# Kernel tuning notes

Hardware: AMD Instinct MI355X
Metric: run time of the kernel (lower is better)

## Reference

```python
import jax, jax.numpy as jnp
import numpy as np

BS, N, K, H = 32, 512, 32, 64

def _lin(k, i, o):
    return jax.random.normal(k, (i, o), jnp.float32) / np.sqrt(i).astype(np.float32)

def setup_inputs() -> dict:
    key = jax.random.key(0)
    ks = jax.random.split(key, 16)
    return {
        "ped_features": jax.random.normal(ks[0], (BS, N, 6), jnp.float32),
        "h_st": jax.random.normal(ks[1], (BS, N, H), jnp.float32),
        "h_neigh": jax.random.normal(ks[2], (BS, N, K, H), jnp.float32),
        "rela_features": jax.random.normal(ks[3], (BS, N, K, 6), jnp.float32),
        "neigh_mask": jax.random.randint(ks[4], (BS, N, K), 0, 2).astype(bool),
        "we1_w": _lin(ks[5], 2 * H + 1, H), "we1_b": jnp.zeros((H,), jnp.float32),
        "we2_w": _lin(ks[6], H, H),         "we2_b": jnp.zeros((H,), jnp.float32),
        "wx1_w": _lin(ks[7], H, H),         "wx1_b": jnp.zeros((H,), jnp.float32),
        "wx2_w": _lin(ks[8], H, 2),         "wx2_b": jnp.zeros((2,), jnp.float32),
        "wa_w":  _lin(ks[9], H, 2),         "wa_b":  jnp.zeros((2,), jnp.float32),
        "wh1_w": _lin(ks[10], 2 * H, H),    "wh1_b": jnp.zeros((H,), jnp.float32),
        "wh2_w": _lin(ks[11], H, H),        "wh2_b": jnp.zeros((H,), jnp.float32),
    }

def reference(ped_features, h_st, h_neigh, rela_features, neigh_mask,
              we1_w, we1_b, we2_w, we2_b,
              wx1_w, wx1_b, wx2_w, wx2_b,
              wa_w, wa_b, wh1_w, wh1_b, wh2_w, wh2_b):
    silu = jax.nn.silu
    # pairwise distances from relative positions  [bs,N,k]
    dists = jnp.sqrt(jnp.sum(rela_features[..., :2] ** 2, axis=-1))
    neigh_num = neigh_mask.sum(axis=-1).astype(h_st.dtype)  # [bs,N]
    # edge features: [h_i repeated, h_j, dist]  -> [bs,N,k,2H+1]
    h_rep = jnp.broadcast_to(h_st[:, :, None, :], (BS, N, K, H))
    tmp = jnp.concatenate([h_rep, h_neigh, dists[..., None]], axis=-1)
    # f_e
    m_ij = silu(silu(tmp @ we1_w + we1_b) @ we2_w + we2_b)  # [bs,N,k,H]
    # f_x -> per-edge 2-vector gates
    fx = silu(silu(m_ij @ wx1_w + wx1_b) @ wx2_w + wx2_b)   # [bs,N,k,2]
    agg = rela_features[..., :2] * fx
    agg = jnp.where(neigh_mask[..., None], agg, 0.0)
    agg = agg.sum(axis=-2) / (neigh_num[..., None] + 1e-6)  # masked mean [bs,N,2]
    # f_a node acceleration update
    a_new = silu(h_st @ wa_w + wa_b) * ped_features[..., 4:] + agg
    v_new = ped_features[..., 2:4] + a_new
    x_new = ped_features[..., :2] + v_new
    # message sum + f_h residual hidden update
    m_i = m_ij.sum(axis=-2)  # [bs,N,H]
    h_new = h_st + (silu(jnp.concatenate([h_st, m_i], axis=-1) @ wh1_w + wh1_b) @ wh2_w + wh2_b)
    return jnp.concatenate([x_new, v_new, a_new], axis=-1), h_new
```

## Files before the change

kernel.cpp:

```cpp
#include <hip/hip_runtime.h>

#define KK 32
#define NODES 16384
#define NPB 16
#define NPWV 4

typedef __bf16 bf16x8 __attribute__((ext_vector_type(8)));
typedef float  f32x4  __attribute__((ext_vector_type(4)));

union FragU { uint4 u; bf16x8 b; unsigned short s[8]; };

__device__ inline float bf2f(unsigned short v) {
    union { unsigned int u; float f; } t; t.u = ((unsigned int)v) << 16; return t.f;
}
__device__ inline unsigned short f2bf(float f) {
    union { float f; unsigned int u; } t; t.f = f;
    unsigned int u = t.u;
    return (unsigned short)((u + 0x7FFFu + ((u >> 16) & 1u)) >> 16);
}
__device__ inline unsigned int pkbf(float a, float b) {
    return (unsigned int)f2bf(a) | ((unsigned int)f2bf(b) << 16);
}
__device__ inline float silu_f(float x) { return x / (1.0f + __expf(-x)); }

__device__ inline float loadf(const void* p, int f32f, int idx) {
    return f32f ? ((const float*)p)[idx] : bf2f(((const unsigned short*)p)[idx]);
}
__device__ inline bf16x8 load8(const void* p, int f32f, int idx) {
    if (f32f) {
        const float* s = (const float*)p + idx;
        float4 lo = *(const float4*)s;
        float4 hi = *(const float4*)(s + 4);
        bf16x8 t;
        t[0] = (__bf16)lo.x; t[1] = (__bf16)lo.y; t[2] = (__bf16)lo.z; t[3] = (__bf16)lo.w;
        t[4] = (__bf16)hi.x; t[5] = (__bf16)hi.y; t[6] = (__bf16)hi.z; t[7] = (__bf16)hi.w;
        return t;
    }
    FragU t; t.u = *(const uint4*)((const unsigned short*)p + idx);
    return t.b;
}
__device__ inline int read_mask(const void* p, int flag, int i) {
    if (flag == 1) return ((const int*)p)[i] != 0;
    if (flag == 0) return ((const unsigned char*)p)[i] != 0;
    if (flag == 2) return ((const unsigned short*)p)[i] != 0;
    return ((const float*)p)[i] != 0.0f;
}
__device__ inline void fence_lds() {
    __builtin_amdgcn_sched_barrier(0);
    __builtin_amdgcn_wave_barrier();
    __builtin_amdgcn_sched_barrier(0);
}

__global__ __launch_bounds__(256, 2) void fused_kernel(
    const void* __restrict__ ped,   const void* __restrict__ h_st,
    const void* __restrict__ h_neigh, const void* __restrict__ rela,
    const void* __restrict__ maskp,
    const void* __restrict__ we1_w, const void* __restrict__ we1_b,
    const void* __restrict__ we2_w, const void* __restrict__ we2_b,
    const void* __restrict__ wx1_w, const void* __restrict__ wx1_b,
    const void* __restrict__ wx2_w, const void* __restrict__ wx2_b,
    const void* __restrict__ wa_w,  const void* __restrict__ wa_b,
    const void* __restrict__ wh1_w, const void* __restrict__ wh1_b,
    const void* __restrict__ wh2_w, const void* __restrict__ wh2_b,
    float* __restrict__ out0, float* __restrict__ out1)
{
    __shared__ uint4 wfr[44][64];
    __shared__ __align__(16) unsigned int lbuf[4][2][16][36];
    __shared__ __align__(16) unsigned int mibuf[16][36];
    __shared__ __align__(16) unsigned int abuf[16][36];
    __shared__ float aggbuf[16][2];
    __shared__ int flagsh[2];

    const int tid  = threadIdx.x;
    const int lane = tid & 63, wv = tid >> 6;
    const int q = lane >> 4, cl = lane & 15;

    if (wv == 0) {
        const unsigned short* hh = (const unsigned short*)h_st;
        bool ok = true;
        #pragma unroll
        for (int t = 0; t < 2; t++) {
            unsigned short v = hh[lane*2 + t];
            if (v) { int e = (v >> 7) & 0xFF; if (e < 90 || e > 165) ok = false; }
        }
        unsigned long long bm = __ballot(ok);
        const unsigned int*   mw = (const unsigned int*)maskp;
        const unsigned short* mh = (const unsigned short*)maskp;
        bool w01 = mw[lane] <= 1u;
        unsigned short h0 = mh[lane*2], h1 = mh[lane*2 + 1];
        bool s16 = (h0 == 0 || h0 == 0x3F80u) && (h1 == 0 || h1 == 0x3F80u);
        bool enz = (h0 != 0);
        unsigned long long bw = __ballot(w01);
        unsigned long long bs = __ballot(s16);
        unsigned long long be = __ballot(enz);
        if (lane == 0) {
            flagsh[1] = (bm == ~0ULL) ? 0 : 1;
            int mf;
            if (bw == ~0ULL) mf = 1;
            else if (bs == ~0ULL) mf = be ? 2 : 3;
            else mf = 0;
            flagsh[0] = mf;
        }
    }
    __syncthreads();
    const int mflag = flagsh[0], f32f = flagsh[1];

    for (int idx = tid; idx < 44*64; idx += 256) {
        int f = idx >> 6, l = idx & 63;
        int lq = l >> 4, ln = l & 15;
        const void *W, *B; int g, klim;
        if (f < 20)      { g = f;      W = we1_w; B = we1_b; klim = 129; }
        else if (f < 32) { g = f - 20; W = we2_w; B = we2_b; klim = 64; }
        else             { g = f - 32; W = wx1_w; B = wx1_b; klim = 64; }
        int ks = g >> 2, nt = g & 3;
        int n = nt*16 + ln;
        FragU fr;
        #pragma unroll
        for (int j = 0; j < 8; j++) {
            int k = ks*32 + lq*8 + j;
            float v = (k < klim) ? loadf(W, f32f, k*64 + n)
                                 : (k == klim ? loadf(B, f32f, n) : 0.0f);
            fr.s[j] = f2bf(v);
        }
        wfr[f][l] = fr.u;
    }
    __syncthreads();

    float wx2r0[4][4], wx2r1[4][4];
    #pragma unroll
    for (int nt = 0; nt < 4; nt++)
        #pragma unroll
        for (int rr = 0; rr < 4; rr++) {
            int frow = nt*16 + q*4 + rr;
            wx2r0[nt][rr] = loadf(wx2_w, f32f, frow*2);
            wx2r1[nt][rr] = loadf(wx2_w, f32f, frow*2 + 1);
        }
    const float bx20 = loadf(wx2_b, f32f, 0), bx21 = loadf(wx2_b, f32f, 1);
    const f32x4 zz = {0.f, 0.f, 0.f, 0.f};

    FragU bc;
    #pragma unroll
    for (int j = 0; j < 8; j++) bc.s[j] = 0;
    if (q == 0) bc.s[0] = 0x3F80u;

    #pragma unroll 1
    for (int it = 0; it < NPWV; ++it) {
        const int node = blockIdx.x*NPB + wv*NPWV + it;

        bf16x8 bst[2];
        #pragma unroll
        for (int ks = 0; ks < 2; ks++)
            bst[ks] = load8(h_st, f32f, node*64 + ks*32 + q*8);
        bf16x8 bng[2][2];
        #pragma unroll
        for (int et = 0; et < 2; et++)
            #pragma unroll
            for (int ks = 0; ks < 2; ks++)
                bng[et][ks] = load8(h_neigh, f32f, (node*KK + et*16 + cl)*64 + ks*32 + q*8);

        float rx[2], ry[2], dv[2]; int mk[2];
        #pragma unroll
        for (int et = 0; et < 2; et++) {
            int e = node*KK + et*16 + cl;
            rx[et] = loadf(rela, f32f, e*6);
            ry[et] = loadf(rela, f32f, e*6 + 1);
            dv[et] = sqrtf(rx[et]*rx[et] + ry[et]*ry[et]);
            mk[et] = read_mask(maskp, mflag, e);
        }
        FragU bext[2];
        #pragma unroll
        for (int et = 0; et < 2; et++) {
            #pragma unroll
            for (int j = 0; j < 8; j++) bext[et].s[j] = 0;
            if (q == 0) { bext[et].s[0] = f2bf(dv[et]); bext[et].s[1] = 0x3F80u; }
        }

        f32x4 acc[2][4];
        #pragma unroll
        for (int et = 0; et < 2; et++)
            #pragma unroll
            for (int nt = 0; nt < 4; nt++) acc[et][nt] = zz;
        #pragma unroll
        for (int ks = 0; ks < 5; ks++) {
            bf16x8 b0 = (ks < 2) ? bst[ks] : (ks < 4 ? bng[0][ks-2] : bext[0].b);
            bf16x8 b1 = (ks < 2) ? bst[ks] : (ks < 4 ? bng[1][ks-2] : bext[1].b);
            #pragma unroll
            for (int nt = 0; nt < 4; nt++) {
                FragU w; w.u = wfr[ks*4 + nt][lane];
                acc[0][nt] = __builtin_amdgcn_mfma_f32_16x16x32_bf16(w.b, b0, acc[0][nt], 0, 0, 0);
                acc[1][nt] = __builtin_amdgcn_mfma_f32_16x16x32_bf16(w.b, b1, acc[1][nt], 0, 0, 0);
            }
        }

        fence_lds();
        #pragma unroll
        for (int et = 0; et < 2; et++)
            #pragma unroll
            for (int nt = 0; nt < 4; nt++) {
                uint2 pr;
                pr.x = pkbf(silu_f(acc[et][nt][0]), silu_f(acc[et][nt][1]));
                pr.y = pkbf(silu_f(acc[et][nt][2]), silu_f(acc[et][nt][3]));
                *(uint2*)&lbuf[wv][et][cl][nt*8 + q*2] = pr;
            }
        fence_lds();

        bf16x8 b2[2][2];
        #pragma unroll
        for (int et = 0; et < 2; et++)
            #pragma unroll
            for (int ks = 0; ks < 2; ks++) {
                FragU t; t.u = *(const uint4*)&lbuf[wv][et][cl][ks*16 + q*4];
                b2[et][ks] = t.b;
            }
        f32x4 mac[2][4];
        #pragma unroll
        for (int et = 0; et < 2; et++)
            #pragma unroll
            for (int nt = 0; nt < 4; nt++) mac[et][nt] = zz;
        #pragma unroll
        for (int ks = 0; ks < 3; ks++) {
            bf16x8 bb0 = (ks < 2) ? b2[0][ks] : bc.b;
            bf16x8 bb1 = (ks < 2) ? b2[1][ks] : bc.b;
            #pragma unroll
            for (int nt = 0; nt < 4; nt++) {
                FragU w; w.u = wfr[20 + ks*4 + nt][lane];
                mac[0][nt] = __builtin_amdgcn_mfma_f32_16x16x32_bf16(w.b, bb0, mac[0][nt], 0, 0, 0);
                mac[1][nt] = __builtin_amdgcn_mfma_f32_16x16x32_bf16(w.b, bb1, mac[1][nt], 0, 0, 0);
            }
        }

        float mip[4][4];
        fence_lds();
        #pragma unroll
        for (int nt = 0; nt < 4; nt++) {
            float v0[2], v1[2], v2[2], v3[2];
            #pragma unroll
            for (int et = 0; et < 2; et++) {
                v0[et] = silu_f(mac[et][nt][0]); v1[et] = silu_f(mac[et][nt][1]);
                v2[et] = silu_f(mac[et][nt][2]); v3[et] = silu_f(mac[et][nt][3]);
                uint2 pr; pr.x = pkbf(v0[et], v1[et]); pr.y = pkbf(v2[et], v3[et]);
                *(uint2*)&lbuf[wv][et][cl][nt*8 + q*2] = pr;
            }
            mip[nt][0] = v0[0] + v0[1]; mip[nt][1] = v1[0] + v1[1];
            mip[nt][2] = v2[0] + v2[1]; mip[nt][3] = v3[0] + v3[1];
        }
        fence_lds();

        bf16x8 b3[2][2];
        #pragma unroll
        for (int et = 0; et < 2; et++)
            #pragma unroll
            for (int ks = 0; ks < 2; ks++) {
                FragU t; t.u = *(const uint4*)&lbuf[wv][et][cl][ks*16 + q*4];
                b3[et][ks] = t.b;
            }
        f32x4 xac[2][4];
        #pragma unroll
        for (int et = 0; et < 2; et++)
            #pragma unroll
            for (int nt = 0; nt < 4; nt++) xac[et][nt] = zz;
        #pragma unroll
        for (int ks = 0; ks < 3; ks++) {
            bf16x8 bb0 = (ks < 2) ? b3[0][ks] : bc.b;
            bf16x8 bb1 = (ks < 2) ? b3[1][ks] : bc.b;
            #pragma unroll
            for (int nt = 0; nt < 4; nt++) {
                FragU w; w.u = wfr[32 + ks*4 + nt][lane];
                xac[0][nt] = __builtin_amdgcn_mfma_f32_16x16x32_bf16(w.b, bb0, xac[0][nt], 0, 0, 0);
                xac[1][nt] = __builtin_amdgcn_mfma_f32_16x16x32_bf16(w.b, bb1, xac[1][nt], 0, 0, 0);
            }
        }

        float p0[2] = {0.f, 0.f}, p1[2] = {0.f, 0.f};
        #pragma unroll
        for (int et = 0; et < 2; et++)
            #pragma unroll
            for (int nt = 0; nt < 4; nt++)
                #pragma unroll
                for (int rr = 0; rr < 4; rr++) {
                    float xv = silu_f(xac[et][nt][rr]);
                    p0[et] += xv * wx2r0[nt][rr];
                    p1[et] += xv * wx2r1[nt][rr];
                }
        float axp = 0.f, ayp = 0.f, cnp = 0.f;
        #pragma unroll
        for (int et = 0; et < 2; et++) {
            p0[et] += __shfl_xor(p0[et], 16); p0[et] += __shfl_xor(p0[et], 32);
            p1[et] += __shfl_xor(p1[et], 16); p1[et] += __shfl_xor(p1[et], 32);
            float f0 = silu_f(p0[et] + bx20), f1 = silu_f(p1[et] + bx21);
            if (mk[et]) { axp += rx[et]*f0; ayp += ry[et]*f1; cnp += 1.0f; }
        }
        #pragma unroll
        for (int m = 1; m < 16; m <<= 1) {
            axp += __shfl_xor(axp, m); ayp += __shfl_xor(ayp, m); cnp += __shfl_xor(cnp, m);
        }
        #pragma unroll
        for (int nt = 0; nt < 4; nt++)
            #pragma unroll
            for (int rr = 0; rr < 4; rr++) {
                float s = mip[nt][rr];
                s += __shfl_xor(s, 1); s += __shfl_xor(s, 2);
                s += __shfl_xor(s, 4); s += __shfl_xor(s, 8);
                mip[nt][rr] = s;
            }
        const int nl = wv*NPWV + it;
        if (cl == 0) {
            #pragma unroll
            for (int nt = 0; nt < 4; nt++) {
                uint2 pr;
                pr.x = pkbf(mip[nt][0], mip[nt][1]);
                pr.y = pkbf(mip[nt][2], mip[nt][3]);
                *(uint2*)&mibuf[nl][nt*8 + q*2] = pr;
            }
            if (q == 0) {
                aggbuf[nl][0] = axp / (cnp + 1e-6f);
                aggbuf[nl][1] = ayp / (cnp + 1e-6f);
            }
        }
    }

    __syncthreads();

    for (int idx = tid; idx < 32*64; idx += 256) {
        int f = idx >> 6, l = idx & 63;
        int lq = l >> 4, ln = l & 15;
        const void *W, *B; int g, klim;
        if (f < 20) { g = f;      W = wh1_w; B = wh1_b; klim = 128; }
        else        { g = f - 20; W = wh2_w; B = wh2_b; klim = 64; }
        int ks = g >> 2, nt = g & 3;
        int n = nt*16 + ln;
        FragU fr;
        #pragma unroll
        for (int j = 0; j < 8; j++) {
            int k = ks*32 + lq*8 + j;
            float v = (k < klim) ? loadf(W, f32f, k*64 + n)
                                 : (k == klim ? loadf(B, f32f, n) : 0.0f);
            fr.s[j] = f2bf(v);
        }
        wfr[f][l] = fr.u;
    }
    __syncthreads();

    const int nb = blockIdx.x*NPB;

    bf16x8 afr[5];
    #pragma unroll
    for (int ks = 0; ks < 2; ks++)
        afr[ks] = load8(h_st, f32f, (nb + cl)*64 + ks*32 + q*8);
    #pragma unroll
    for (int ks = 2; ks < 4; ks++) {
        FragU t; t.u = *(const uint4*)&mibuf[cl][(ks-2)*16 + q*4];
        afr[ks] = t.b;
    }
    afr[4] = bc.b;

    f32x4 hacc = zz;
    #pragma unroll
    for (int ks = 0; ks < 5; ks++) {
        FragU w; w.u = wfr[ks*4 + wv][lane];
        hacc = __builtin_amdgcn_mfma_f32_16x16x32_bf16(afr[ks], w.b, hacc, 0, 0, 0);
    }
    {
        unsigned short* ab = (unsigned short*)abuf;
        #pragma unroll
        for (int rr = 0; rr < 4; rr++)
            ab[(q*4 + rr)*72 + wv*16 + cl] = f2bf(silu_f(hacc[rr]));
    }
    __syncthreads();

    bf16x8 a2[3];
    #pragma unroll
    for (int ks = 0; ks < 2; ks++) {
        FragU t; t.u = *(const uint4*)&abuf[cl][ks*16 + q*4];
        a2[ks] = t.b;
    }
    a2[2] = bc.b;
    f32x4 h2 = zz;
    #pragma unroll
    for (int ks = 0; ks < 3; ks++) {
        FragU w; w.u = wfr[20 + ks*4 + wv][lane];
        h2 = __builtin_amdgcn_mfma_f32_16x16x32_bf16(a2[ks], w.b, h2, 0, 0, 0);
    }
    #pragma unroll
    for (int rr = 0; rr < 4; rr++) {
        int row = nb + q*4 + rr, col = wv*16 + cl;
        out1[row*64 + col] = loadf(h_st, f32f, row*64 + col) + h2[rr];
    }

    if (wv == 0) {
        FragU bwa[2];
        #pragma unroll
        for (int ks = 0; ks < 2; ks++) {
            #pragma unroll
            for (int j = 0; j < 8; j++)
                bwa[ks].s[j] = (cl < 2) ? f2bf(loadf(wa_w, f32f, (ks*32 + q*8 + j)*2 + cl)) : 0;
        }
        f32x4 sac = zz;
        #pragma unroll
        for (int ks = 0; ks < 2; ks++)
            sac = __builtin_amdgcn_mfma_f32_16x16x32_bf16(afr[ks], bwa[ks].b, sac, 0, 0, 0);
        if (cl < 2) {
            int j = cl;
            float wb = loadf(wa_b, f32f, j);
            #pragma unroll
            for (int rr = 0; rr < 4; rr++) {
                int row = q*4 + rr, gnode = nb + row;
                float a = silu_f(sac[rr] + wb) * loadf(ped, f32f, gnode*6 + 4 + j)
                          + aggbuf[row][j];
                float v = loadf(ped, f32f, gnode*6 + 2 + j) + a;
                float x = loadf(ped, f32f, gnode*6 + j) + v;
                out0[gnode*6 + j]     = x;
                out0[gnode*6 + 2 + j] = v;
                out0[gnode*6 + 4 + j] = a;
            }
        }
    }
}

extern "C" void kernel_launch(void* const* d_in, const int* in_sizes, int n_in,
                              void* d_out, int out_size, void* d_ws, size_t ws_size,
                              hipStream_t stream) {
    float* out0 = (float*)d_out;
    float* out1 = out0 + (size_t)NODES*6;
    fused_kernel<<<NODES/NPB, 256, 0, stream>>>(
        d_in[0], d_in[1], d_in[2], d_in[3], d_in[4],
        d_in[5], d_in[6], d_in[7], d_in[8],
        d_in[9], d_in[10], d_in[11], d_in[12],
        d_in[13], d_in[14], d_in[15], d_in[16], d_in[17], d_in[18],
        out0, out1);
}
```

Measured before the change: 332.0 us.

## Fold biases and distance term into epilogues, drop extra MFMA K-steps

Removes the extra K-slice that encoded biases and the distance feature through MFMA, applying them instead as per-lane scalar adds and FMAs in the silu epilogues, with the constants held as packed bf16 registers. This cuts the MFMA count per layer and shrinks the weight fragment LDS buffer. It also swaps silu and the division for hardware exp2/rcp intrinsics, uses native bf16 conversion, and raises launch bounds to 3 blocks per CU by reusing LDS buffers. The costs are extra VALU work per output element, more register pressure from the packed constants, and slightly different rounding because the bias and distance terms are now added in fp32.

Result: slower. 377.1 us (+13.6%).

```diff
diff --git a/kernel.cpp b/kernel.cpp
--- a/kernel.cpp
+++ b/kernel.cpp
@@ -8,21 +8,27 @@
 typedef __bf16 bf16x8 __attribute__((ext_vector_type(8)));
 typedef float  f32x4  __attribute__((ext_vector_type(4)));
 
-union FragU { uint4 u; bf16x8 b; unsigned short s[8]; };
+union FragU { uint4 u; bf16x8 b; unsigned short s[8]; __bf16 h[8]; };
 
 __device__ inline float bf2f(unsigned short v) {
     union { unsigned int u; float f; } t; t.u = ((unsigned int)v) << 16; return t.f;
 }
-__device__ inline unsigned short f2bf(float f) {
-    union { float f; unsigned int u; } t; t.f = f;
-    unsigned int u = t.u;
-    return (unsigned short)((u + 0x7FFFu + ((u >> 16) & 1u)) >> 16);
+__device__ inline unsigned short sbf(float f) {
+    union { __bf16 h; unsigned short s; } t; t.h = (__bf16)f; return t.s;
 }
 __device__ inline unsigned int pkbf(float a, float b) {
-    return (unsigned int)f2bf(a) | ((unsigned int)f2bf(b) << 16);
-}
-__device__ inline float silu_f(float x) { return x / (1.0f + __expf(-x)); }
-
+    union { unsigned int u; __bf16 h[2]; } r;
+    r.h[0] = (__bf16)a; r.h[1] = (__bf16)b; return r.u;
+}
+__device__ inline float upk(unsigned int u, int hi) {
+    union { unsigned int v; float f; } t;
+    t.v = hi ? (u & 0xFFFF0000u) : (u << 16);
+    return t.f;
+}
+__device__ inline float silu_f(float x) {
+    float e = __builtin_amdgcn_exp2f(-1.44269504f * x);
+    return x * __builtin_amdgcn_rcpf(1.0f + e);
+}
 __device__ inline float loadf(const void* p, int f32f, int idx) {
     return f32f ? ((const float*)p)[idx] : bf2f(((const unsigned short*)p)[idx]);
 }
@@ -31,10 +37,10 @@
         const float* s = (const float*)p + idx;
         float4 lo = *(const float4*)s;
         float4 hi = *(const float4*)(s + 4);
-        bf16x8 t;
-        t[0] = (__bf16)lo.x; t[1] = (__bf16)lo.y; t[2] = (__bf16)lo.z; t[3] = (__bf16)lo.w;
-        t[4] = (__bf16)hi.x; t[5] = (__bf16)hi.y; t[6] = (__bf16)hi.z; t[7] = (__bf16)hi.w;
-        return t;
+        FragU t;
+        t.h[0] = (__bf16)lo.x; t.h[1] = (__bf16)lo.y; t.h[2] = (__bf16)lo.z; t.h[3] = (__bf16)lo.w;
+        t.h[4] = (__bf16)hi.x; t.h[5] = (__bf16)hi.y; t.h[6] = (__bf16)hi.z; t.h[7] = (__bf16)hi.w;
+        return t.b;
     }
     FragU t; t.u = *(const uint4*)((const unsigned short*)p + idx);
     return t.b;
@@ -51,7 +57,7 @@
     __builtin_amdgcn_sched_barrier(0);
 }
 
-__global__ __launch_bounds__(256, 2) void fused_kernel(
+__global__ __launch_bounds__(256, 3) void fused_kernel(
     const void* __restrict__ ped,   const void* __restrict__ h_st,
     const void* __restrict__ h_neigh, const void* __restrict__ rela,
     const void* __restrict__ maskp,
@@ -64,10 +70,9 @@
     const void* __restrict__ wh2_w, const void* __restrict__ wh2_b,
     float* __restrict__ out0, float* __restrict__ out1)
 {
-    __shared__ uint4 wfr[44][64];
-    __shared__ __align__(16) unsigned int lbuf[4][2][16][36];
-    __shared__ __align__(16) unsigned int mibuf[16][36];
-    __shared__ __align__(16) unsigned int abuf[16][36];
+    __shared__ uint4 wfr[32][64];
+    __shared__ __align__(16) unsigned int lbuf[4][2][576];
+    __shared__ __align__(16) unsigned int mibuf[576];
     __shared__ float aggbuf[16][2];
     __shared__ int flagsh[2];
 
@@ -105,43 +110,38 @@
     __syncthreads();
     const int mflag = flagsh[0], f32f = flagsh[1];
 
-    for (int idx = tid; idx < 44*64; idx += 256) {
+    for (int idx = tid; idx < 32*64; idx += 256) {
         int f = idx >> 6, l = idx & 63;
         int lq = l >> 4, ln = l & 15;
-        const void *W, *B; int g, klim;
-        if (f < 20)      { g = f;      W = we1_w; B = we1_b; klim = 129; }
-        else if (f < 32) { g = f - 20; W = we2_w; B = we2_b; klim = 64; }
-        else             { g = f - 32; W = wx1_w; B = wx1_b; klim = 64; }
+        const void* W; int g;
+        if (f < 16)      { W = we1_w; g = f; }
+        else if (f < 24) { W = we2_w; g = f - 16; }
+        else             { W = wx1_w; g = f - 24; }
         int ks = g >> 2, nt = g & 3;
-        int n = nt*16 + ln;
+        int k0 = ks*32 + lq*8, n = nt*16 + ln;
         FragU fr;
         #pragma unroll
-        for (int j = 0; j < 8; j++) {
-            int k = ks*32 + lq*8 + j;
-            float v = (k < klim) ? loadf(W, f32f, k*64 + n)
-                                 : (k == klim ? loadf(B, f32f, n) : 0.0f);
-            fr.s[j] = f2bf(v);
-        }
+        for (int j = 0; j < 8; j++)
+            fr.s[j] = sbf(loadf(W, f32f, (k0 + j)*64 + n));
         wfr[f][l] = fr.u;
     }
     __syncthreads();
 
-    float wx2r0[4][4], wx2r1[4][4];
+    unsigned int cb[6][4][2];
     #pragma unroll
     for (int nt = 0; nt < 4; nt++)
         #pragma unroll
-        for (int rr = 0; rr < 4; rr++) {
-            int frow = nt*16 + q*4 + rr;
-            wx2r0[nt][rr] = loadf(wx2_w, f32f, frow*2);
-            wx2r1[nt][rr] = loadf(wx2_w, f32f, frow*2 + 1);
+        for (int pr = 0; pr < 2; pr++) {
+            int f0 = nt*16 + q*4 + pr*2, f1 = f0 + 1;
+            cb[0][nt][pr] = pkbf(loadf(we1_b, f32f, f0),          loadf(we1_b, f32f, f1));
+            cb[1][nt][pr] = pkbf(loadf(we1_w, f32f, 128*64 + f0), loadf(we1_w, f32f, 128*64 + f1));
+            cb[2][nt][pr] = pkbf(loadf(we2_b, f32f, f0),          loadf(we2_b, f32f, f1));
+            cb[3][nt][pr] = pkbf(loadf(wx1_b, f32f, f0),          loadf(wx1_b, f32f, f1));
+            cb[4][nt][pr] = pkbf(loadf(wx2_w, f32f, f0*2),        loadf(wx2_w, f32f, f1*2));
+            cb[5][nt][pr] = pkbf(loadf(wx2_w, f32f, f0*2 + 1),    loadf(wx2_w, f32f, f1*2 + 1));
         }
     const float bx20 = loadf(wx2_b, f32f, 0), bx21 = loadf(wx2_b, f32f, 1);
     const f32x4 zz = {0.f, 0.f, 0.f, 0.f};
-
-    FragU bc;
-    #pragma unroll
-    for (int j = 0; j < 8; j++) bc.s[j] = 0;
-    if (q == 0) bc.s[0] = 0x3F80u;
 
     #pragma unroll 1
     for (int it = 0; it < NPWV; ++it) {
@@ -167,13 +167,6 @@
             dv[et] = sqrtf(rx[et]*rx[et] + ry[et]*ry[et]);
             mk[et] = read_mask(maskp, mflag, e);
         }
-        FragU bext[2];
-        #pragma unroll
-        for (int et = 0; et < 2; et++) {
-            #pragma unroll
-            for (int j = 0; j < 8; j++) bext[et].s[j] = 0;
-            if (q == 0) { bext[et].s[0] = f2bf(dv[et]); bext[et].s[1] = 0x3F80u; }
-        }
 
         f32x4 acc[2][4];
         #pragma unroll
@@ -181,9 +174,9 @@
             #pragma unroll
             for (int nt = 0; nt < 4; nt++) acc[et][nt] = zz;
         #pragma unroll
-        for (int ks = 0; ks < 5; ks++) {
-            bf16x8 b0 = (ks < 2) ? bst[ks] : (ks < 4 ? bng[0][ks-2] : bext[0].b);
-            bf16x8 b1 = (ks < 2) ? bst[ks] : (ks < 4 ? bng[1][ks-2] : bext[1].b);
+        for (int ks = 0; ks < 4; ks++) {
+            bf16x8 b0 = (ks < 2) ? bst[ks] : bng[0][ks-2];
+            bf16x8 b1 = (ks < 2) ? bst[ks] : bng[1][ks-2];
             #pragma unroll
             for (int nt = 0; nt < 4; nt++) {
                 FragU w; w.u = wfr[ks*4 + nt][lane];
@@ -198,9 +191,11 @@
             #pragma unroll
             for (int nt = 0; nt < 4; nt++) {
                 uint2 pr;
-                pr.x = pkbf(silu_f(acc[et][nt][0]), silu_f(acc[et][nt][1]));
-                pr.y = pkbf(silu_f(acc[et][nt][2]), silu_f(acc[et][nt][3]));
-                *(uint2*)&lbuf[wv][et][cl][nt*8 + q*2] = pr;
+                pr.x = pkbf(silu_f(acc[et][nt][0] + upk(cb[0][nt][0],0) + dv[et]*upk(cb[1][nt][0],0)),
+                            silu_f(acc[et][nt][1] + upk(cb[0][nt][0],1) + dv[et]*upk(cb[1][nt][0],1)));
+                pr.y = pkbf(silu_f(acc[et][nt][2] + upk(cb[0][nt][1],0) + dv[et]*upk(cb[1][nt][1],0)),
+                            silu_f(acc[et][nt][3] + upk(cb[0][nt][1],1) + dv[et]*upk(cb[1][nt][1],1)));
+                *(uint2*)&lbuf[wv][et][cl*36 + nt*8 + q*2] = pr;
             }
         fence_lds();
 
@@ -209,7 +204,7 @@
         for (int et = 0; et < 2; et++)
             #pragma unroll
             for (int ks = 0; ks < 2; ks++) {
-                FragU t; t.u = *(const uint4*)&lbuf[wv][et][cl][ks*16 + q*4];
+                FragU t; t.u = *(const uint4*)&lbuf[wv][et][cl*36 + ks*16 + q*4];
                 b2[et][ks] = t.b;
             }
         f32x4 mac[2][4];
@@ -218,31 +213,30 @@
             #pragma unroll
             for (int nt = 0; nt < 4; nt++) mac[et][nt] = zz;
         #pragma unroll
-        for (int ks = 0; ks < 3; ks++) {
-            bf16x8 bb0 = (ks < 2) ? b2[0][ks] : bc.b;
-            bf16x8 bb1 = (ks < 2) ? b2[1][ks] : bc.b;
+        for (int ks = 0; ks < 2; ks++)
             #pragma unroll
             for (int nt = 0; nt < 4; nt++) {
-                FragU w; w.u = wfr[20 + ks*4 + nt][lane];
-                mac[0][nt] = __builtin_amdgcn_mfma_f32_16x16x32_bf16(w.b, bb0, mac[0][nt], 0, 0, 0);
-                mac[1][nt] = __builtin_amdgcn_mfma_f32_16x16x32_bf16(w.b, bb1, mac[1][nt], 0, 0, 0);
-            }
-        }
+                FragU w; w.u = wfr[16 + ks*4 + nt][lane];
+                mac[0][nt] = __builtin_amdgcn_mfma_f32_16x16x32_bf16(w.b, b2[0][ks], mac[0][nt], 0, 0, 0);
+                mac[1][nt] = __builtin_amdgcn_mfma_f32_16x16x32_bf16(w.b, b2[1][ks], mac[1][nt], 0, 0, 0);
+            }
 
         float mip[4][4];
         fence_lds();
         #pragma unroll
         for (int nt = 0; nt < 4; nt++) {
-            float v0[2], v1[2], v2[2], v3[2];
+            float v[4][2];
             #pragma unroll
             for (int et = 0; et < 2; et++) {
-                v0[et] = silu_f(mac[et][nt][0]); v1[et] = silu_f(mac[et][nt][1]);
-                v2[et] = silu_f(mac[et][nt][2]); v3[et] = silu_f(mac[et][nt][3]);
-                uint2 pr; pr.x = pkbf(v0[et], v1[et]); pr.y = pkbf(v2[et], v3[et]);
-                *(uint2*)&lbuf[wv][et][cl][nt*8 + q*2] = pr;
-            }
-            mip[nt][0] = v0[0] + v0[1]; mip[nt][1] = v1[0] + v1[1];
-            mip[nt][2] = v2[0] + v2[1]; mip[nt][3] = v3[0] + v3[1];
+                v[0][et] = silu_f(mac[et][nt][0] + upk(cb[2][nt][0],0));
+                v[1][et] = silu_f(mac[et][nt][1] + upk(cb[2][nt][0],1));
+                v[2][et] = silu_f(mac[et][nt][2] + upk(cb[2][nt][1],0));
+                v[3][et] = silu_f(mac[et][nt][3] + upk(cb[2][nt][1],1));
+                uint2 pr; pr.x = pkbf(v[0][et], v[1][et]); pr.y = pkbf(v[2][et], v[3][et]);
+                *(uint2*)&lbuf[wv][et][cl*36 + nt*8 + q*2] = pr;
+            }
+            #pragma unroll
+            for (int rr = 0; rr < 4; rr++) mip[nt][rr] = v[rr][0] + v[rr][1];
         }
         fence_lds();
 
@@ -251,7 +245,7 @@
         for (int et = 0; et < 2; et++)
             #pragma unroll
             for (int ks = 0; ks < 2; ks++) {
-                FragU t; t.u = *(const uint4*)&lbuf[wv][et][cl][ks*16 + q*4];
+                FragU t; t.u = *(const uint4*)&lbuf[wv][et][cl*36 + ks*16 + q*4];
                 b3[et][ks] = t.b;
             }
         f32x4 xac[2][4];
@@ -260,16 +254,13 @@
             #pragma unroll
             for (int nt = 0; nt < 4; nt++) xac[et][nt] = zz;
         #pragma unroll
-        for (int ks = 0; ks < 3; ks++) {
-            bf16x8 bb0 = (ks < 2) ? b3[0][ks] : bc.b;
-            bf16x8 bb1 = (ks < 2) ? b3[1][ks] : bc.b;
+        for (int ks = 0; ks < 2; ks++)
             #pragma unroll
             for (int nt = 0; nt < 4; nt++) {
-                FragU w; w.u = wfr[32 + ks*4 + nt][lane];
-                xac[0][nt] = __builtin_amdgcn_mfma_f32_16x16x32_bf16(w.b, bb0, xac[0][nt], 0, 0, 0);
-                xac[1][nt] = __builtin_amdgcn_mfma_f32_16x16x32_bf16(w.b, bb1, xac[1][nt], 0, 0, 0);
-            }
-        }
+                FragU w; w.u = wfr[24 + ks*4 + nt][lane];
+                xac[0][nt] = __builtin_amdgcn_mfma_f32_16x16x32_bf16(w.b, b3[0][ks], xac[0][nt], 0, 0, 0);
+                xac[1][nt] = __builtin_amdgcn_mfma_f32_16x16x32_bf16(w.b, b3[1][ks], xac[1][nt], 0, 0, 0);
+            }
 
         float p0[2] = {0.f, 0.f}, p1[2] = {0.f, 0.f};
         #pragma unroll
@@ -278,9 +269,9 @@
             for (int nt = 0; nt < 4; nt++)
                 #pragma unroll
                 for (int rr = 0; rr < 4; rr++) {
-                    float xv = silu_f(xac[et][nt][rr]);
-                    p0[et] += xv * wx2r0[nt][rr];
-                    p1[et] += xv * wx2r1[nt][rr];
+                    float xv = silu_f(xac[et][nt][rr] + upk(cb[3][nt][rr>>1], rr&1));
+                    p0[et] += xv * upk(cb[4][nt][rr>>1], rr&1);
+                    p1[et] += xv * upk(cb[5][nt][rr>>1], rr&1);
                 }
         float axp = 0.f, ayp = 0.f, cnp = 0.f;
         #pragma unroll
@@ -310,81 +301,77 @@
                 uint2 pr;
                 pr.x = pkbf(mip[nt][0], mip[nt][1]);
                 pr.y = pkbf(mip[nt][2], mip[nt][3]);
-                *(uint2*)&mibuf[nl][nt*8 + q*2] = pr;
+                *(uint2*)&mibuf[nl*36 + nt*8 + q*2] = pr;
             }
             if (q == 0) {
-                aggbuf[nl][0] = axp / (cnp + 1e-6f);
-                aggbuf[nl][1] = ayp / (cnp + 1e-6f);
+                float rc = __builtin_amdgcn_rcpf(cnp + 1e-6f);
+                aggbuf[nl][0] = axp * rc;
+                aggbuf[nl][1] = ayp * rc;
             }
         }
     }
 
     __syncthreads();
 
-    for (int idx = tid; idx < 32*64; idx += 256) {
+    for (int idx = tid; idx < 24*64; idx += 256) {
         int f = idx >> 6, l = idx & 63;
         int lq = l >> 4, ln = l & 15;
-        const void *W, *B; int g, klim;
-        if (f < 20) { g = f;      W = wh1_w; B = wh1_b; klim = 128; }
-        else        { g = f - 20; W = wh2_w; B = wh2_b; klim = 64; }
+        const void* W; int g;
+        if (f < 16) { W = wh1_w; g = f; }
+        else        { W = wh2_w; g = f - 16; }
         int ks = g >> 2, nt = g & 3;
-        int n = nt*16 + ln;
+        int k0 = ks*32 + lq*8, n = nt*16 + ln;
         FragU fr;
         #pragma unroll
-        for (int j = 0; j < 8; j++) {
-            int k = ks*32 + lq*8 + j;
-            float v = (k < klim) ? loadf(W, f32f, k*64 + n)
-                                 : (k == klim ? loadf(B, f32f, n) : 0.0f);
-            fr.s[j] = f2bf(v);
-        }
+        for (int j = 0; j < 8; j++)
+            fr.s[j] = sbf(loadf(W, f32f, (k0 + j)*64 + n));
         wfr[f][l] = fr.u;
     }
     __syncthreads();
 
+    const float bh1v = loadf(wh1_b, f32f, wv*16 + cl);
+    const float bh2v = loadf(wh2_b, f32f, wv*16 + cl);
     const int nb = blockIdx.x*NPB;
 
-    bf16x8 afr[5];
+    bf16x8 afr[4];
     #pragma unroll
     for (int ks = 0; ks < 2; ks++)
         afr[ks] = load8(h_st, f32f, (nb + cl)*64 + ks*32 + q*8);
     #pragma unroll
     for (int ks = 2; ks < 4; ks++) {
-        FragU t; t.u = *(const uint4*)&mibuf[cl][(ks-2)*16 + q*4];
+        FragU t; t.u = *(const uint4*)&mibuf[cl*36 + (ks-2)*16 + q*4];
         afr[ks] = t.b;
     }
-    afr[4] = bc.b;
 
     f32x4 hacc = zz;
     #pragma unroll
-    for (int ks = 0; ks < 5; ks++) {
+    for (int ks = 0; ks < 4; ks++) {
         FragU w; w.u = wfr[ks*4 + wv][lane];
         hacc = __builtin_amdgcn_mfma_f32_16x16x32_bf16(afr[ks], w.b, hacc, 0, 0, 0);
     }
-    {
-        unsigned short* ab = (unsigned short*)abuf;
-        #pragma unroll
-        for (int rr = 0; rr < 4; rr++)
-            ab[(q*4 + rr)*72 + wv*16 + cl] = f2bf(silu_f(hacc[rr]));
-    }
+    unsigned short* ab = (unsigned short*)lbuf;
+    #pragma unroll
+    for (int rr = 0; rr < 4; rr++)
+        ab[(q*4 + rr)*72 + wv*16 + cl] = sbf(silu_f(hacc[rr] + bh1v));
     __syncthreads();
 
-    bf16x8 a2[3];
+    bf16x8 a2[2];
+    const unsigned int* ab32 = (const unsigned int*)lbuf;
     #pragma unroll
     for (int ks = 0; ks < 2; ks++) {
-        FragU t; t.u = *(const uint4*)&abuf[cl][ks*16 + q*4];
+        FragU t; t.u = *(const uint4*)&ab32[cl*36 + ks*16 + q*4];
         a2[ks] = t.b;
     }
-    a2[2] = bc.b;
     f32x4 h2 = zz;
     #pragma unroll
-    for (int ks = 0; ks < 3; ks++) {
-        FragU w; w.u = wfr[20 + ks*4 + wv][lane];
+    for (int ks = 0; ks < 2; ks++) {
+        FragU w; w.u = wfr[16 + ks*4 + wv][lane];
         h2 = __builtin_amdgcn_mfma_f32_16x16x32_bf16(a2[ks], w.b, h2, 0, 0, 0);
     }
     #pragma unroll
     for (int rr = 0; rr < 4; rr++) {
         int row = nb + q*4 + rr, col = wv*16 + cl;
-        out1[row*64 + col] = loadf(h_st, f32f, row*64 + col) + h2[rr];
+        out1[row*64 + col] = loadf(h_st, f32f, row*64 + col) + h2[rr] + bh2v;
     }
 
     if (wv == 0) {
@@ -393,7 +380,7 @@
         for (int ks = 0; ks < 2; ks++) {
             #pragma unroll
             for (int j = 0; j < 8; j++)
-                bwa[ks].s[j] = (cl < 2) ? f2bf(loadf(wa_w, f32f, (ks*32 + q*8 + j)*2 + cl)) : 0;
+                bwa[ks].s[j] = (cl < 2) ? sbf(loadf(wa_w, f32f, (ks*32 + q*8 + j)*2 + cl)) : 0;
         }
         f32x4 sac = zz;
         #pragma unroll
```
